# Optimization experiments

Measured on AMD Instinct MI355X. Metric: run time of the kernel, lower is better.

Reference implementation:

```python
import jax, jax.numpy as jnp
import numpy as np

B, G, S, GS, P = 32, 512, 128, 32, 10
C, H, RED = 384, 6, 16
HID = 4 * C
D = C // H
SCALE = D ** -0.5

def _gelu(x):
    return jax.nn.gelu(x, approximate=False)

def _ln(x, g, b):
    m = jnp.mean(x, -1, keepdims=True)
    v = jnp.var(x, -1, keepdims=True)
    return (x - m) * jax.lax.rsqrt(v + 1e-5) * g + b

def _split_qkv(x, W):
    Bn, T, Cc = x.shape
    qkv = (x @ W).reshape(Bn, T, 3, H, D).transpose(2, 0, 3, 1, 4)
    return qkv[0], qkv[1], qkv[2]

def _merge(x):
    Bn, Hh, T, Dd = x.shape
    return x.transpose(0, 2, 1, 3).reshape(Bn, T, Hh * Dd)

def _mha(q, k, v):
    a = jax.nn.softmax(jnp.einsum('bhnd,bhmd->bhnm', q, k) * SCALE, axis=-1)
    return jnp.einsum('bhnm,bhmd->bhnd', a, v)

def _forward(x, center1, center2, neighborhood, prompt_embeddings, ln1_g, ln1_b, Wqkv, Wproj, bproj, gate, ln2_g, ln2_b, W1, b1, W2, b2, ad_down_W, ad_down_b, ad_up_W, ad_up_b, ad_gate, bn_g, bn_b, bn_mean, bn_var, ln3_g, ln3_b, a1_Wqkv, a1_Wproj, a1_bproj, ad1_down_W, ad1_down_b, ad1_up_W, ad1_up_b, idx, center_idx, group_size, if_maxmean, pro_cof, center_cof):
    Bx, Ntok, Cc = x.shape
    # prompt dropout is identity in eval
    prompt = jnp.broadcast_to(prompt_embeddings, (Bx, P, Cc))
    # --- gated dual self / prompt-cross attention ---
    xn = _ln(x, ln1_g, ln1_b)
    q, k, v = _split_qkv(xn, Wqkv)
    xs = _mha(q, k, v)                                  # [B,H,N,D]
    _, pk, pv = _split_qkv(prompt, Wqkv)
    pa = jax.nn.softmax(jnp.einsum('bhnd,bhpd->bhnp', q, pk) * SCALE, axis=-1)
    px = jnp.einsum('bhnp,bhpd->bhnd', gate * pa, pv)   # learned gate per head
    x = x + (_merge(xs) + _merge(px)) @ Wproj + bproj
    # --- MLP + gated bottleneck adapter residual ---
    h = _gelu(_ln(x, ln2_g, ln2_b) @ W1 + b1) @ W2 + b2
    h_ad = h + _gelu(h @ ad_down_W + ad_down_b) @ ad_up_W + ad_up_b
    x = ad_gate * h_ad + x
    cls_x = x[:, :1]
    xt = x[:, 1:]                                       # [B,G,C]
    flat = xt.reshape(Bx * G, Cc)
    x_nb = flat[idx].reshape(Bx * S, group_size, Cc)    # KNN neighborhoods
    x_ct = flat[center_idx].reshape(Bx, S, Cc)          # center features
    # NOTE: original normalizes `neighborhood` by its std, but result is unused
    # --- local self-attention (attn1 over norm3) on each neighborhood ---
    nq, nk, nv = _split_qkv(_ln(x_nb, ln3_g, ln3_b), a1_Wqkv)
    no = _mha(nq, nk, nv)
    x_nb = x_nb + _merge(no) @ a1_Wproj + a1_bproj
    knn = x_nb.reshape(Bx, S, group_size, Cc)
    lc = jnp.max(knn, axis=2)
    if if_maxmean:
        lc = lc + jnp.mean(knn, axis=2)
    # BatchNorm1d (eval, running stats) + GELU over channel dim
    lc = _gelu((lc - bn_mean) * jax.lax.rsqrt(bn_var + 1e-5) * bn_g + bn_b)
    vis = lc + center_cof * x_ct                        # [B,S,C]
    # --- propagate: de_neighbors == S so sorted-topk == full weighted sum ---
    d = jnp.sum((center1[:, :, None, :] - center2[:, None, :, :]) ** 2, axis=-1)  # [B,G,S]
    w = 1.0 / (d + 1e-8)
    w = w / jnp.sum(w, axis=-1, keepdims=True)
    interp = jnp.einsum('bns,bsc->bnc', w, vis)
    xt = xt + pro_cof * interp
    out = jnp.concatenate([cls_x, xt], axis=1)
    # adapter1
    out = out + _gelu(out @ ad1_down_W + ad1_down_b) @ ad1_up_W + ad1_up_b
    return out

def setup_inputs():
    ks = jax.random.split(jax.random.key(0), 20)
    r = lambda i, shape, s=0.02: jax.random.normal(ks[i], shape, jnp.float32) * s
    return {
        'x': jax.random.normal(ks[0], (B, G + 1, C), jnp.float32),
        'center1': jax.random.normal(ks[1], (B, G, 3), jnp.float32),
        'center2': jax.random.normal(ks[2], (B, S, 3), jnp.float32),
        'neighborhood': jax.random.normal(ks[3], (B, S, GS, 3), jnp.float32),
        'prompt_embeddings': r(4, (P, C)),
        'ln1_g': jnp.ones(C), 'ln1_b': jnp.zeros(C),
        'Wqkv': r(5, (C, 3 * C)),
        'Wproj': r(6, (C, C)), 'bproj': jnp.zeros(C),
        'gate': jax.random.normal(ks[7], (1, H, 1, 1), jnp.float32),
        'ln2_g': jnp.ones(C), 'ln2_b': jnp.zeros(C),
        'W1': r(8, (C, HID)), 'b1': jnp.zeros(HID),
        'W2': r(9, (HID, C)), 'b2': jnp.zeros(C),
        'ad_down_W': r(10, (C, RED)), 'ad_down_b': jnp.zeros(RED),
        'ad_up_W': r(11, (RED, C)), 'ad_up_b': jnp.zeros(C),
        'ad_gate': jax.random.normal(ks[12], (), jnp.float32),
        'bn_g': jnp.ones(C), 'bn_b': jnp.zeros(C),
        'bn_mean': jnp.zeros(C), 'bn_var': jnp.ones(C),
        'ln3_g': jnp.ones(C), 'ln3_b': jnp.zeros(C),
        'a1_Wqkv': r(13, (C, 3 * C)),
        'a1_Wproj': r(14, (C, C)), 'a1_bproj': jnp.zeros(C),
        'ad1_down_W': r(15, (C, RED)), 'ad1_down_b': jnp.zeros(RED),
        'ad1_up_W': r(16, (RED, C)), 'ad1_up_b': jnp.zeros(C),
        'idx': jax.random.randint(ks[17], (B * S * GS,), 0, B * G),
        'center_idx': jax.random.randint(ks[18], (B * S,), 0, B * G),
        'group_size': GS,
        'if_maxmean': 1,
        'pro_cof': 1,
        'center_cof': 1,
    }

def reference(x, center1, center2, neighborhood, prompt_embeddings, ln1_g, ln1_b, Wqkv, Wproj, bproj, gate, ln2_g, ln2_b, W1, b1, W2, b2, ad_down_W, ad_down_b, ad_up_W, ad_up_b, ad_gate, bn_g, bn_b, bn_mean, bn_var, ln3_g, ln3_b, a1_Wqkv, a1_Wproj, a1_bproj, ad1_down_W, ad1_down_b, ad1_up_W, ad1_up_b, idx, center_idx, group_size, if_maxmean, pro_cof, center_cof):
    return _forward(x, center1, center2, neighborhood, prompt_embeddings, ln1_g, ln1_b, Wqkv, Wproj, bproj, gate, ln2_g, ln2_b, W1, b1, W2, b2, ad_down_W, ad_down_b, ad_up_W, ad_up_b, ad_gate, bn_g, bn_b, bn_mean, bn_var, ln3_g, ln3_b, a1_Wqkv, a1_Wproj, a1_bproj, ad1_down_W, ad1_down_b, ad1_up_W, ad1_up_b, idx, center_idx, group_size, if_maxmean, pro_cof, center_cof)
```

## Files before the change

kernel.cpp:

```cpp
#include <hip/hip_runtime.h>
#include <hip/hip_bf16.h>
#include <cstdint>
#include <cstddef>

typedef __hip_bfloat16 bf16;
constexpr int TOK = 32 * 513;

typedef __attribute__((ext_vector_type(8))) short short8;
typedef __attribute__((ext_vector_type(4))) float f32x4;

__device__ __forceinline__ float bflo(unsigned u){ return __uint_as_float(u << 16); }
__device__ __forceinline__ float bfhi(unsigned u){ return __uint_as_float(u & 0xffff0000u); }
__device__ __forceinline__ float b2f(bf16 x){ return __bfloat162float(x); }
__device__ __forceinline__ bf16  f2b(float x){ return __float2bfloat16(x); }
__device__ __forceinline__ float geluf(float x){ return 0.5f*x*(1.0f + erff(x*0.70710678118654752f)); }
__device__ __forceinline__ void unp8(uint4 u, float* f){
  f[0]=bflo(u.x); f[1]=bfhi(u.x); f[2]=bflo(u.y); f[3]=bfhi(u.y);
  f[4]=bflo(u.z); f[5]=bfhi(u.z); f[6]=bflo(u.w); f[7]=bfhi(u.w);
}
__device__ __forceinline__ float scal(const int* p){
  const int i = *p;
  if (i > -1000000 && i < 1000000) return (float)i;
  return __int_as_float(i);
}
__device__ __forceinline__ f32x4 mfma16(short8 a, short8 b, f32x4 c){
  return __builtin_amdgcn_mfma_f32_16x16x32_bf16(a, b, c, 0, 0, 0);
}
__device__ __forceinline__ int swzl(int l){ return l ^ ((l >> 3) & 7); }

__global__ __launch_bounds__(256) void detect_kernel(const unsigned* __restrict__ x,
                                                     int* __restrict__ flag)
{
  const int t = threadIdx.x;
  bool bad = false;
  for (int i = t; i < 2048; i += 256){
    const unsigned u = x[i];
    const float a = fabsf(bflo(u)), b = fabsf(bfhi(u));
    if (!(a < 1e6f) || !(b < 1e6f)) bad = true;
  }
  __shared__ int s;
  if (t == 0) s = 0;
  __syncthreads();
  const unsigned long long m = __ballot(bad);
  if (m != 0ull && (t & 63) == 0) atomicOr(&s, 1);
  __syncthreads();
  if (t == 0) *flag = s;
}

struct ConvArgs {
  const void* src[34];
  bf16*       dst[34];
  int         n[34];
};
__global__ __launch_bounds__(256) void convert_many(const int* __restrict__ flag, ConvArgs a)
{
  const int ii = blockIdx.y;
  const bool isf = (*flag != 0);
  const int n = a.n[ii];
  const void* s = a.src[ii];
  bf16* d = a.dst[ii];
  for (int i = blockIdx.x*256 + threadIdx.x; i < n; i += gridDim.x*256){
    d[i] = isf ? f2b(((const float*)s)[i]) : ((const bf16*)s)[i];
  }
}

__global__ __launch_bounds__(256) void shuffle_b(const bf16* __restrict__ W,
    bf16* __restrict__ out, int N, int KT, int NT)
{
  const int id = blockIdx.x*256 + threadIdx.x;
  if (id >= NT*KT*64) return;
  const int l  = id & 63;
  const int k0 = (id >> 6) % KT;
  const int n0 = (id >> 6) / KT;
  bf16 tmp[8];
  #pragma unroll
  for (int j = 0; j < 8; j++)
    tmp[j] = W[(size_t)(k0*32 + (l>>4)*8 + j)*N + n0*16 + (l&15)];
  *(uint4*)(out + (size_t)id*8) = *(const uint4*)tmp;
}

template<bool SRC_BF16>
__global__ __launch_bounds__(256) void ln_kernel(const void* __restrict__ src,
    const bf16* __restrict__ g, const bf16* __restrict__ b,
    bf16* __restrict__ out, int rows)
{
  const int wave = (blockIdx.x * blockDim.x + threadIdx.x) >> 6;
  const int lane = threadIdx.x & 63;
  if (wave >= rows) return;
  float v[6]; float s = 0.f, s2 = 0.f;
  #pragma unroll
  for (int i = 0; i < 6; i++){
    const int c = lane + 64*i;
    float x;
    if (SRC_BF16) x = b2f(((const bf16*)src)[(size_t)wave*384 + c]);
    else          x = ((const float*)src)[(size_t)wave*384 + c];
    v[i] = x; s += x; s2 += x*x;
  }
  #pragma unroll
  for (int mm = 32; mm; mm >>= 1){ s += __shfl_xor(s, mm); s2 += __shfl_xor(s2, mm); }
  const float mean = s * (1.f/384.f);
  const float rs = rsqrtf(s2 * (1.f/384.f) - mean*mean + 1e-5f);
  #pragma unroll
  for (int i = 0; i < 6; i++){
    const int c = lane + 64*i;
    out[(size_t)wave*384 + c] = f2b((v[i]-mean)*rs*b2f(g[c]) + b2f(b[c]));
  }
}

__global__ __launch_bounds__(256) void ln3_kernel(const float* __restrict__ xres,
    const bf16* __restrict__ g, const bf16* __restrict__ b, bf16* __restrict__ out)
{
  const int r = (blockIdx.x * blockDim.x + threadIdx.x) >> 6;
  const int lane = threadIdx.x & 63;
  if (r >= 16384) return;
  const int tok = (r >> 9)*513 + 1 + (r & 511);
  const float* xp = xres + (size_t)tok*384;
  float v[6]; float s = 0.f, s2 = 0.f;
  #pragma unroll
  for (int i = 0; i < 6; i++){
    const float x = xp[lane + 64*i];
    v[i] = x; s += x; s2 += x*x;
  }
  #pragma unroll
  for (int mm = 32; mm; mm >>= 1){ s += __shfl_xor(s, mm); s2 += __shfl_xor(s2, mm); }
  const float mean = s * (1.f/384.f);
  const float rs = rsqrtf(s2 * (1.f/384.f) - mean*mean + 1e-5f);
  #pragma unroll
  for (int i = 0; i < 6; i++){
    const int c = lane + 64*i;
    out[(size_t)r*384 + c] = f2b((v[i]-mean)*rs*b2f(g[c]) + b2f(b[c]));
  }
}

template<int EPI>
__global__ __launch_bounds__(256) void mfma_gemm(
    const bf16* __restrict__ A, const bf16* __restrict__ Bsh,
    const bf16* __restrict__ bias, const bf16* __restrict__ resid,
    void* __restrict__ outv, int M, int N, int K)
{
  __shared__ __align__(16) bf16 sA[8*64*8];
  const int t = threadIdx.x, lane = t & 63, w = t >> 6;
  const int l15 = lane & 15, quad = lane >> 4;
  const int wm = w & 1, wn = w >> 1;
  const int m0 = blockIdx.y * 128;
  const int n0t = blockIdx.x * 8 + wn * 4;
  const int KT = K >> 5;
  f32x4 acc[4][4];
  #pragma unroll
  for (int i = 0; i < 4; i++){
    #pragma unroll
    for (int j = 0; j < 4; j++) acc[i][j] = f32x4{0.f,0.f,0.f,0.f};
  }
  const int arow = t >> 1, ac0 = (t & 1) * 16;
  const int amt = arow >> 4, al15 = arow & 15, aq0 = (ac0 >> 3);

  for (int ks = 0; ks < KT; ks++){
    uint4 u0 = {0,0,0,0}, u1 = {0,0,0,0};
    const int gm = m0 + arow;
    if (gm < M){
      const bf16* ap = A + (size_t)gm*K + ks*32 + ac0;
      u0 = *(const uint4*)ap; u1 = *(const uint4*)(ap + 8);
    }
    *(uint4*)(sA + ((amt*64 + aq0*16     + al15) << 3)) = u0;
    *(uint4*)(sA + ((amt*64 + (aq0+1)*16 + al15) << 3)) = u1;
    __syncthreads();
    short8 afr[4];
    #pragma unroll
    for (int i = 0; i < 4; i++)
      afr[i] = *(const short8*)(sA + (((wm*4+i)*64 + lane) << 3));
    #pragma unroll
    for (int j = 0; j < 4; j++){
      const short8 b = *(const short8*)(Bsh + ((size_t)((n0t+j)*KT + ks)*64 + lane)*8);
      #pragma unroll
      for (int i = 0; i < 4; i++) acc[i][j] = mfma16(afr[i], b, acc[i][j]);
    }
    __syncthreads();
  }
  #pragma unroll
  for (int i = 0; i < 4; i++){
    #pragma unroll
    for (int r = 0; r < 4; r++){
      const int gm = m0 + (wm*4+i)*16 + quad*4 + r;
      if (gm < M){
        #pragma unroll
        for (int j = 0; j < 4; j++){
          const int gn = (n0t+j)*16 + l15;
          float v = acc[i][j][r];
          const size_t o = (size_t)gm*N + gn;
          if (EPI == 0){ v += b2f(bias[gn]); ((bf16*)outv)[o] = f2b(v); }
          else if (EPI == 1){ ((bf16*)outv)[o] = f2b(v); }
          else if (EPI == 2){ v += b2f(bias[gn]); ((bf16*)outv)[o] = f2b(geluf(v)); }
          else { v += b2f(bias[gn]) + b2f(resid[o]); ((float*)outv)[o] = v; }
        }
      }
    }
  }
}

__global__ __launch_bounds__(256) void pqkv_kernel(const bf16* __restrict__ pe,
    const bf16* __restrict__ Wqkv, float* __restrict__ pq)
{
  const int n  = blockIdx.x*64 + (threadIdx.x & 63);
  const int rg = threadIdx.x >> 6;
  for (int r = rg; r < 10; r += 4){
    float s0 = 0.f, s1 = 0.f;
    for (int c = 0; c < 384; c += 2){
      s0 = fmaf(b2f(pe[(size_t)r*384+c]),   b2f(Wqkv[(size_t)c*1152 + n]),     s0);
      s1 = fmaf(b2f(pe[(size_t)r*384+c+1]), b2f(Wqkv[(size_t)(c+1)*1152 + n]), s1);
    }
    pq[(size_t)r*1152 + n] = s0 + s1;
  }
}

__global__ __launch_bounds__(256) void attn_kernel(
    const bf16* __restrict__ qkv, const float* __restrict__ pq,
    const bf16* __restrict__ gate, bf16* __restrict__ ao)
{
  __shared__ __align__(16) bf16 s_q[64*72];
  __shared__ __align__(16) bf16 s_k[64*72];
  __shared__ __align__(16) bf16 s_vT[64*72];
  __shared__ __align__(16) bf16 s_p[4*16*40];
  __shared__ __align__(16) bf16 s_pk[16*72];
  __shared__ __align__(16) bf16 s_pvT[64*40];
  const int bh = blockIdx.y;
  const int b = bh / 6, h = bh % 6;
  const int q0 = blockIdx.x * 64;
  const int t = threadIdx.x, lane = t & 63, w = t >> 6;
  const int l15 = lane & 15, quad = lane >> 4;

  {
    const int row = t >> 2, dc = (t & 3) * 16;
    const int tok = q0 + row;
    uint4 u0 = {0,0,0,0}, u1 = {0,0,0,0};
    if (tok < 513){
      const bf16* p = qkv + (size_t)(b*513 + tok)*1152 + h*64 + dc;
      u0 = *(const uint4*)p; u1 = *(const uint4*)(p + 8);
    }
    *(uint4*)(s_q + row*72 + dc)     = u0;
    *(uint4*)(s_q + row*72 + dc + 8) = u1;
  }
  {
    const int j = t >> 4, dc = (t & 15) * 4;
    float f[4] = {0.f,0.f,0.f,0.f};
    if (j < 10){
      const float* pk = pq + (size_t)j*1152 + 384 + h*64 + dc;
      f[0]=pk[0]; f[1]=pk[1]; f[2]=pk[2]; f[3]=pk[3];
    }
    bf16 tmp[4] = {f2b(f[0]),f2b(f[1]),f2b(f[2]),f2b(f[3])};
    *(uint2*)(s_pk + j*72 + dc) = *(const uint2*)tmp;
  }
  {
    const int d = t & 63, kg = t >> 6;
    #pragma unroll
    for (int kk = 0; kk < 8; kk++){
      const int key = kg*8 + kk;
      bf16 v = f2b(0.f);
      if (key < 10) v = f2b(pq[(size_t)key*1152 + 768 + h*64 + d]);
      s_pvT[d*40 + key] = v;
    }
  }

  float m_i[4], l_i[4];
  f32x4 oacc[4];
  #pragma unroll
  for (int r = 0; r < 4; r++){ m_i[r] = -30000.f; l_i[r] = 0.f; }
  #pragma unroll
  for (int nt = 0; nt < 4; nt++) oacc[nt] = f32x4{0.f,0.f,0.f,0.f};
  bf16* myp = s_p + w*16*40;
  const short8* aq = (const short8*)(s_q + (w*16 + l15)*72);

  for (int kt = 0; kt < 9; kt++){
    const int kb = kt*64;
    __syncthreads();
    {
      const int kp = t & 31, dg = t >> 5;
      const int key0 = kb + 2*kp;
      uint4 k0v = {0,0,0,0}, k1v = {0,0,0,0}, v0 = {0,0,0,0}, v1 = {0,0,0,0};
      if (key0 < 513){
        const bf16* base = qkv + (size_t)(b*513 + key0)*1152 + h*64 + dg*8;
        k0v = *(const uint4*)(base + 384);
        v0  = *(const uint4*)(base + 768);
      }
      if (key0 + 1 < 513){
        const bf16* base = qkv + (size_t)(b*513 + key0 + 1)*1152 + h*64 + dg*8;
        k1v = *(const uint4*)(base + 384);
        v1  = *(const uint4*)(base + 768);
      }
      *(uint4*)(s_k + (2*kp)*72   + dg*8) = k0v;
      *(uint4*)(s_k + (2*kp+1)*72 + dg*8) = k1v;
      const unsigned short* a0 = (const unsigned short*)&v0;
      const unsigned short* a1 = (const unsigned short*)&v1;
      unsigned* vt = (unsigned*)s_vT;
      #pragma unroll
      for (int j = 0; j < 8; j++)
        vt[(dg*8 + j)*36 + kp] = (unsigned)a0[j] | ((unsigned)a1[j] << 16);
    }
    __syncthreads();

    f32x4 sreg[4];
    #pragma unroll
    for (int nt = 0; nt < 4; nt++){
      f32x4 acc = f32x4{0.f,0.f,0.f,0.f};
      const short8* bk = (const short8*)(s_k + (nt*16 + l15)*72);
      acc = mfma16(aq[quad],     bk[quad],     acc);
      acc = mfma16(aq[4 + quad], bk[4 + quad], acc);
      const bool kvalid = (kb + nt*16 + l15) < 513;
      #pragma unroll
      for (int r = 0; r < 4; r++)
        sreg[nt][r] = kvalid ? acc[r]*0.125f : -30000.f;
    }
    float alpha[4];
    #pragma unroll
    for (int r = 0; r < 4; r++){
      float mx = fmaxf(fmaxf(sreg[0][r], sreg[1][r]), fmaxf(sreg[2][r], sreg[3][r]));
      #pragma unroll
      for (int mm = 8; mm; mm >>= 1) mx = fmaxf(mx, __shfl_xor(mx, mm));
      const float mn = fmaxf(m_i[r], mx);
      alpha[r] = __expf(m_i[r] - mn);
      m_i[r] = mn;
      float ps = 0.f;
      #pragma unroll
      for (int nt = 0; nt < 4; nt++){
        const float p = __expf(sreg[nt][r] - mn);
        sreg[nt][r] = p; ps += p;
      }
      #pragma unroll
      for (int mm = 8; mm; mm >>= 1) ps += __shfl_xor(ps, mm);
      l_i[r] = l_i[r]*alpha[r] + ps;
    }
    #pragma unroll
    for (int nt = 0; nt < 4; nt++){
      #pragma unroll
      for (int r = 0; r < 4; r++)
        myp[(quad*4 + r)*40 + nt*16 + l15] = f2b(sreg[nt][r]);
    }
    #pragma unroll
    for (int nt = 0; nt < 4; nt++){
      #pragma unroll
      for (int r = 0; r < 4; r++) oacc[nt][r] *= alpha[r];
    }
    const short8* ap = (const short8*)(myp + l15*40);
    #pragma unroll
    for (int nt = 0; nt < 4; nt++){
      const short8* bv = (const short8*)(s_vT + (nt*16 + l15)*72);
      oacc[nt] = mfma16(ap[quad],     bv[quad],     oacc[nt]);
      oacc[nt] = mfma16(ap[4 + quad], bv[4 + quad], oacc[nt]);
    }
  }

  f32x4 sp;
  {
    f32x4 acc = f32x4{0.f,0.f,0.f,0.f};
    const short8* bp = (const short8*)(s_pk + l15*72);
    acc = mfma16(aq[quad],     bp[quad],     acc);
    acc = mfma16(aq[4 + quad], bp[4 + quad], acc);
    #pragma unroll
    for (int r = 0; r < 4; r++)
      sp[r] = (l15 < 10) ? acc[r]*0.125f : -30000.f;
  }
  float psr[4];
  #pragma unroll
  for (int r = 0; r < 4; r++){
    float mx = sp[r];
    #pragma unroll
    for (int mm = 8; mm; mm >>= 1) mx = fmaxf(mx, __shfl_xor(mx, mm));
    const float p = __expf(sp[r] - mx);
    float ps = p;
    #pragma unroll
    for (int mm = 8; mm; mm >>= 1) ps += __shfl_xor(ps, mm);
    psr[r] = ps;
    myp[(quad*4 + r)*40 + l15]      = f2b(p);
    myp[(quad*4 + r)*40 + 16 + l15] = f2b(0.f);
  }
  f32x4 pva[4];
  {
    const short8* ap = (const short8*)(myp + l15*40);
    #pragma unroll
    for (int nt = 0; nt < 4; nt++){
      const short8* bv = (const short8*)(s_pvT + (nt*16 + l15)*40);
      pva[nt] = mfma16(ap[quad], bv[quad], f32x4{0.f,0.f,0.f,0.f});
    }
  }

  const float gh = b2f(gate[h]);
  #pragma unroll
  for (int r = 0; r < 4; r++){
    const int tok = q0 + w*16 + quad*4 + r;
    if (tok < 513){
      const float invl = 1.f/l_i[r];
      const float gps  = gh/psr[r];
      #pragma unroll
      for (int nt = 0; nt < 4; nt++){
        const float val = oacc[nt][r]*invl + pva[nt][r]*gps;
        ao[(size_t)(b*513 + tok)*384 + h*64 + nt*16 + l15] = f2b(val);
      }
    }
  }
}

__global__ __launch_bounds__(256) void adapter_mid_kernel(const bf16* __restrict__ h,
    const bf16* __restrict__ Wd, const bf16* __restrict__ bd,
    const bf16* __restrict__ Wu, const bf16* __restrict__ bu,
    const bf16* __restrict__ p_gate, float* __restrict__ xres)
{
  __shared__ float s_h[384];
  __shared__ float s_part[16][17];
  __shared__ float s_y[16];
  const size_t row = blockIdx.x;
  const int t = threadIdx.x;
  const bf16* hp = h + row*384;
  for (int c = t; c < 384; c += 256) s_h[c] = b2f(hp[c]);
  __syncthreads();
  const int o = t & 15, p = t >> 4;
  float part0 = 0.f, part1 = 0.f;
  for (int c = p; c < 384; c += 32){
    part0 = fmaf(s_h[c],    b2f(Wd[(size_t)c*16 + o]),      part0);
    part1 = fmaf(s_h[c+16], b2f(Wd[(size_t)(c+16)*16 + o]), part1);
  }
  s_part[o][p] = part0 + part1;
  __syncthreads();
  if (t < 16){
    float sum = 0.f;
    #pragma unroll
    for (int pp = 0; pp < 16; pp++) sum += s_part[t][pp];
    s_y[t] = geluf(sum + b2f(bd[t]));
  }
  __syncthreads();
  const float g = b2f(p_gate[0]);
  for (int c = t; c < 384; c += 256){
    float up = 0.f;
    #pragma unroll
    for (int o2 = 0; o2 < 16; o2++) up = fmaf(s_y[o2], b2f(Wu[(size_t)o2*384 + c]), up);
    const float had = s_h[c] + up + b2f(bu[c]);
    xres[row*384 + c] = g*had + xres[row*384 + c];
  }
}

__global__ __launch_bounds__(256) void adapter_final_kernel(const float* __restrict__ xr,
    const bf16* __restrict__ Wd, const bf16* __restrict__ bd,
    const bf16* __restrict__ Wu, const bf16* __restrict__ bu,
    const int* __restrict__ flag, void* __restrict__ out)
{
  __shared__ float s_h[384];
  __shared__ float s_part[16][17];
  __shared__ float s_y[16];
  const size_t row = blockIdx.x;
  const int t = threadIdx.x;
  const float* hp = xr + row*384;
  for (int c = t; c < 384; c += 256) s_h[c] = hp[c];
  __syncthreads();
  const int o = t & 15, p = t >> 4;
  float part0 = 0.f, part1 = 0.f;
  for (int c = p; c < 384; c += 32){
    part0 = fmaf(s_h[c],    b2f(Wd[(size_t)c*16 + o]),      part0);
    part1 = fmaf(s_h[c+16], b2f(Wd[(size_t)(c+16)*16 + o]), part1);
  }
  s_part[o][p] = part0 + part1;
  __syncthreads();
  if (t < 16){
    float sum = 0.f;
    #pragma unroll
    for (int pp = 0; pp < 16; pp++) sum += s_part[t][pp];
    s_y[t] = geluf(sum + b2f(bd[t]));
  }
  __syncthreads();
  const bool isf = (*flag != 0);
  for (int c = t; c < 384; c += 256){
    float up = 0.f;
    #pragma unroll
    for (int o2 = 0; o2 < 16; o2++) up = fmaf(s_y[o2], b2f(Wu[(size_t)o2*384 + c]), up);
    const float v = s_h[c] + up + b2f(bu[c]);
    if (isf) ((float*)out)[row*384 + c] = v;
    else     ((bf16*)out)[row*384 + c] = f2b(v);
  }
}

__global__ __launch_bounds__(512) void local_kernel(
    const bf16* __restrict__ qkv3, const float* __restrict__ xres,
    const int* __restrict__ idx, const int* __restrict__ cidx,
    const bf16* __restrict__ Bp, const bf16* __restrict__ bp1,
    const bf16* __restrict__ bng, const bf16* __restrict__ bnb,
    const bf16* __restrict__ bnm, const bf16* __restrict__ bnv,
    const int* __restrict__ p_ifmm, const int* __restrict__ p_ccof,
    float* __restrict__ vis)
{
  __shared__ __align__(16) bf16 sQ[6*4*64*8];
  __shared__ __align__(16) bf16 sK[6*4*64*8];
  __shared__ __align__(16) bf16 sV[6*4*64*8];
  __shared__ __align__(16) bf16 sP[2*64*8];
  __shared__ __align__(16) bf16 sO[4*64*8];
  __shared__ int s_flat[32];
  __shared__ int s_tok[32];

  const int g = blockIdx.x;
  const int t = threadIdx.x, lane = t & 63, w = t >> 6;
  const int l15 = lane & 15, quad = lane >> 4;
  const int lanez = swzl(lane);

  if (t < 32){
    const int r = idx[g*32 + t];
    s_flat[t] = r;
    s_tok[t]  = (r >> 9)*513 + 1 + (r & 511);
  }
  __syncthreads();

  for (int ch = t; ch < 4608; ch += 512){
    const int row = ch & 31;
    const int c0  = (ch >> 5) * 8;
    const uint4 u = *(const uint4*)(qkv3 + (size_t)s_flat[row]*1152 + c0);
    const int grp = c0 / 384;
    const int rem = c0 - grp*384;
    const int h = rem >> 6, d0 = rem & 63;
    if (grp < 2){
      const int T = h*4 + (row>>4)*2 + (d0>>5);
      const int L = ((d0>>3)&3)*16 + (row&15);
      const int addr = (T*64 + swzl(L))*8;
      if (grp == 0) *(uint4*)(sQ + addr) = u;
      else          *(uint4*)(sK + addr) = u;
    } else {
      const bf16* sv = (const bf16*)&u;
      #pragma unroll
      for (int j2 = 0; j2 < 8; j2++){
        const int d = d0 + j2;
        const int L = (row>>3)*16 + (d&15);
        sV[((h*4 + (d>>4))*64 + swzl(L))*8 + (row&7)] = sv[j2];
      }
    }
  }
  __syncthreads();

  f32x4 accp[3][2];
  #pragma unroll
  for (int a = 0; a < 3; a++){
    #pragma unroll
    for (int m = 0; m < 2; m++) accp[a][m] = f32x4{0.f,0.f,0.f,0.f};
  }

  for (int h = 0; h < 6; h++){
    if (w < 2){
      const int mt = w;
      f32x4 sr[2];
      #pragma unroll
      for (int nt = 0; nt < 2; nt++){
        f32x4 acc = f32x4{0.f,0.f,0.f,0.f};
        #pragma unroll
        for (int k0 = 0; k0 < 2; k0++){
          const short8 a = *(const short8*)(sQ + ((h*4 + mt*2 + k0)*64 + lanez)*8);
          const short8 b = *(const short8*)(sK + ((h*4 + nt*2 + k0)*64 + lanez)*8);
          acc = mfma16(a, b, acc);
        }
        #pragma unroll
        for (int r = 0; r < 4; r++) sr[nt][r] = acc[r]*0.125f;
      }
      #pragma unroll
      for (int r = 0; r < 4; r++){
        float mx = fmaxf(sr[0][r], sr[1][r]);
        #pragma unroll
        for (int mm = 8; mm; mm >>= 1) mx = fmaxf(mx, __shfl_xor(mx, mm));
        const float e0 = __expf(sr[0][r] - mx), e1 = __expf(sr[1][r] - mx);
        float sm = e0 + e1;
        #pragma unroll
        for (int mm = 8; mm; mm >>= 1) sm += __shfl_xor(sm, mm);
        const float inv = 1.f/sm;
        const int m = quad*4 + r;
        const int L0 = (l15 >> 3)*16       + m;
        const int L1 = (2 + (l15 >> 3))*16 + m;
        sP[(mt*64 + swzl(L0))*8 + (l15 & 7)] = f2b(e0*inv);
        sP[(mt*64 + swzl(L1))*8 + (l15 & 7)] = f2b(e1*inv);
      }
    }
    __syncthreads();

    {
      const int mt = w & 1, nt = w >> 1;
      const short8 a = *(const short8*)(sP + (mt*64 + lanez)*8);
      const short8 b = *(const short8*)(sV + ((h*4 + nt)*64 + lanez)*8);
      const f32x4 o = mfma16(a, b, f32x4{0.f,0.f,0.f,0.f});
      const int k0w = nt >> 1, qdw = (nt & 1)*2 + (l15 >> 3), jw = l15 & 7;
      #pragma unroll
      for (int r = 0; r < 4; r++){
        const int L = qdw*16 + quad*4 + r;
        sO[((mt*2 + k0w)*64 + swzl(L))*8 + jw] = f2b(o[r]);
      }
    }
    __syncthreads();

    {
      short8 afr[2][2];
      #pragma unroll
      for (int mt = 0; mt < 2; mt++){
        #pragma unroll
        for (int k0l = 0; k0l < 2; k0l++)
          afr[mt][k0l] = *(const short8*)(sO + ((mt*2 + k0l)*64 + lanez)*8);
      }
      #pragma unroll
      for (int tt = 0; tt < 3; tt++){
        const int nt = w*3 + tt;
        #pragma unroll
        for (int k0l = 0; k0l < 2; k0l++){
          const short8 b = *(const short8*)(Bp + ((size_t)(nt*12 + 2*h + k0l)*64 + lane)*8);
          accp[tt][0] = mfma16(afr[0][k0l], b, accp[tt][0]);
          accp[tt][1] = mfma16(afr[1][k0l], b, accp[tt][1]);
        }
      }
    }
    __syncthreads();
  }

  const float fmm  = scal(p_ifmm);
  const float ccof = scal(p_ccof);
  const int cr = cidx[g];
  const int ctok = (cr >> 9)*513 + 1 + (cr & 511);
  #pragma unroll
  for (int tt = 0; tt < 3; tt++){
    const int n = (w*3 + tt)*16 + l15;
    const float bb = b2f(bp1[n]);
    float mx = -3e30f, sm = 0.f;
    #pragma unroll
    for (int mt = 0; mt < 2; mt++){
      #pragma unroll
      for (int r = 0; r < 4; r++){
        const int tok = mt*16 + quad*4 + r;
        const float v = accp[tt][mt][r] + bb + xres[(size_t)s_tok[tok]*384 + n];
        mx = fmaxf(mx, v); sm += v;
      }
    }
    mx = fmaxf(mx, __shfl_xor(mx, 16)); sm += __shfl_xor(sm, 16);
    mx = fmaxf(mx, __shfl_xor(mx, 32)); sm += __shfl_xor(sm, 32);
    if (quad == 0){
      const float lc = (fmm != 0.f) ? (mx + sm*(1.f/32.f)) : mx;
      const float nr = (lc - b2f(bnm[n])) * rsqrtf(b2f(bnv[n]) + 1e-5f) * b2f(bng[n]) + b2f(bnb[n]);
      vis[(size_t)g*384 + n] = geluf(nr) + ccof * xres[(size_t)ctok*384 + n];
    }
  }
}

__global__ __launch_bounds__(256) void interp_kernel(const bf16* __restrict__ c1,
    const bf16* __restrict__ c2, const float* __restrict__ vis,
    const int* __restrict__ p_pcof, float* __restrict__ xres)
{
  __shared__ float s_w[8][128];
  __shared__ float s_red[2];
  const int b = blockIdx.y;
  const int n0 = blockIdx.x * 8;
  const int t = threadIdx.x;
  for (int ni = 0; ni < 8; ni++){
    const int n = n0 + ni;
    float wv = 0.f;
    if (t < 128){
      float d2 = 0.f;
      #pragma unroll
      for (int k = 0; k < 3; k++){
        const float a = b2f(c1[((size_t)b*512 + n)*3 + k]);
        const float c = b2f(c2[((size_t)b*128 + t)*3 + k]);
        const float df = a - c; d2 += df*df;
      }
      wv = 1.f/(d2 + 1e-8f);
    }
    float rsum = wv;
    #pragma unroll
    for (int mm = 32; mm; mm >>= 1) rsum += __shfl_xor(rsum, mm);
    if (((t & 63) == 0) && t < 128) s_red[t >> 6] = rsum;
    __syncthreads();
    const float tot = s_red[0] + s_red[1];
    if (t < 128) s_w[ni][t] = wv / tot;
    __syncthreads();
  }
  float acc1[8], acc2[8];
  #pragma unroll
  for (int ni = 0; ni < 8; ni++){ acc1[ni] = 0.f; acc2[ni] = 0.f; }
  for (int s = 0; s < 128; s++){
    const float* vp = vis + ((size_t)b*128 + s)*384;
    const float v1 = vp[t];
    const float v2 = (t < 128) ? vp[t + 256] : 0.f;
    #pragma unroll
    for (int ni = 0; ni < 8; ni++){
      const float wn = s_w[ni][s];
      acc1[ni] = fmaf(wn, v1, acc1[ni]);
      acc2[ni] = fmaf(wn, v2, acc2[ni]);
    }
  }
  const float pc = scal(p_pcof);
  #pragma unroll
  for (int ni = 0; ni < 8; ni++){
    const int tok = b*513 + 1 + n0 + ni;
    xres[(size_t)tok*384 + t] += pc*acc1[ni];
    if (t < 128) xres[(size_t)tok*384 + t + 256] += pc*acc2[ni];
  }
}

extern "C" void kernel_launch(void* const* d_in, const int* in_sizes, int n_in,
                              void* d_out, int out_size, void* d_ws, size_t ws_size,
                              hipStream_t stream)
{
  (void)n_in; (void)out_size; (void)ws_size;
  const int*  idx   = (const int*)d_in[35];
  const int*  cidx  = (const int*)d_in[36];
  const int*  ifmm  = (const int*)d_in[38];
  const int*  pcof  = (const int*)d_in[39];
  const int*  ccof  = (const int*)d_in[40];

  size_t off = 0;
  auto alloc = [&](size_t bytes) -> void* {
    void* p = (char*)d_ws + off; off += (bytes + 255) & ~(size_t)255; return p;
  };
  int*   flag = (int*)  alloc(sizeof(int));
  float* xres = (float*)alloc((size_t)TOK*384*4);
  bf16*  slab = (bf16*) alloc((size_t)TOK*1536*2);
  bf16*  xn   = (bf16*) alloc((size_t)TOK*384*2);
  float* pq   = (float*)alloc((size_t)10*1152*4);
  bf16*  Bq   = (bf16*) alloc((size_t)72*12*64*8*2);
  bf16*  Bp   = (bf16*) alloc((size_t)24*12*64*8*2);
  bf16*  Bqkv = (bf16*) alloc((size_t)72*12*64*8*2);
  bf16*  Bw1  = (bf16*) alloc((size_t)96*12*64*8*2);
  bf16*  Bw2  = (bf16*) alloc((size_t)24*48*64*8*2);
  bf16*  Bwp  = (bf16*) alloc((size_t)24*12*64*8*2);

  bf16*  qkvb = slab;
  bf16*  x_c  = slab + (size_t)TOK*1152;
  bf16*  h1   = slab;
  bf16*  qkv3 = slab;
  bf16*  xln3 = slab + (size_t)TOK*1152;
  bf16*  ao   = xn;
  bf16*  hbuf = xn;
  float* visb = (float*)xn;

  const int conv_ids[34] = {0,1,2,4,5,6,7,8,9,10,11,12,13,14,15,16,17,
                            18,19,20,21,22,23,24,25,26,27,28,29,30,31,32,33,34};
  ConvArgs ca;
  bf16* canon[41];
  int maxn = 1;
  for (int k = 0; k < 34; k++){
    const int i = conv_ids[k];
    const int n = in_sizes[i];
    bf16* dst = (i == 0) ? x_c : (bf16*)alloc((size_t)n*2);
    ca.src[k] = d_in[i]; ca.dst[k] = dst; ca.n[k] = n;
    canon[i] = dst;
    if (n > maxn) maxn = n;
  }
  detect_kernel<<<dim3(1), dim3(256), 0, stream>>>((const unsigned*)d_in[0], flag);
  {
    int gx = (maxn + 256*64 - 1) / (256*64); if (gx > 64) gx = 64; if (gx < 1) gx = 1;
    convert_many<<<dim3(gx, 34), dim3(256), 0, stream>>>(flag, ca);
  }

  const bf16 *x_in = canon[0], *c1 = canon[1], *c2 = canon[2], *pe = canon[4],
             *ln1g = canon[5], *ln1b = canon[6], *Wqkv = canon[7], *Wproj = canon[8],
             *bproj = canon[9], *gate = canon[10], *ln2g = canon[11], *ln2b = canon[12],
             *W1 = canon[13], *b1 = canon[14], *W2 = canon[15], *b2v = canon[16],
             *adW = canon[17], *adb = canon[18], *adU = canon[19], *adub = canon[20],
             *adg = canon[21], *bng = canon[22], *bnb = canon[23], *bnm = canon[24],
             *bnv = canon[25], *ln3g = canon[26], *ln3b = canon[27], *a1W = canon[28],
             *a1P = canon[29], *a1pb = canon[30], *d1W = canon[31], *d1b = canon[32],
             *u1W = canon[33], *u1b = canon[34];

  shuffle_b<<<dim3(216), dim3(256), 0, stream>>>(a1W, Bq, 1152, 12, 72);
  shuffle_b<<<dim3(72),  dim3(256), 0, stream>>>(a1P, Bp, 384, 12, 24);
  shuffle_b<<<dim3(216), dim3(256), 0, stream>>>(Wqkv, Bqkv, 1152, 12, 72);
  shuffle_b<<<dim3(288), dim3(256), 0, stream>>>(W1, Bw1, 1536, 12, 96);
  shuffle_b<<<dim3(288), dim3(256), 0, stream>>>(W2, Bw2, 384, 48, 24);
  shuffle_b<<<dim3(72),  dim3(256), 0, stream>>>(Wproj, Bwp, 384, 12, 24);

  ln_kernel<true><<<dim3((TOK*64)/256), dim3(256), 0, stream>>>((const void*)x_in, ln1g, ln1b, xn, TOK);
  mfma_gemm<1><<<dim3(9,129), dim3(256), 0, stream>>>(xn, Bqkv, nullptr, nullptr, qkvb, TOK, 1152, 384);
  pqkv_kernel<<<dim3(18), dim3(256), 0, stream>>>(pe, Wqkv, pq);
  attn_kernel<<<dim3(9,192), dim3(256), 0, stream>>>(qkvb, pq, gate, ao);
  mfma_gemm<3><<<dim3(3,129), dim3(256), 0, stream>>>(ao, Bwp, bproj, x_in, xres, TOK, 384, 384);
  ln_kernel<false><<<dim3((TOK*64)/256), dim3(256), 0, stream>>>((const void*)xres, ln2g, ln2b, xn, TOK);
  mfma_gemm<2><<<dim3(12,129), dim3(256), 0, stream>>>(xn, Bw1, b1, nullptr, h1, TOK, 1536, 384);
  mfma_gemm<0><<<dim3(3,129), dim3(256), 0, stream>>>(h1, Bw2, b2v, nullptr, hbuf, TOK, 384, 1536);
  adapter_mid_kernel<<<dim3(TOK), dim3(256), 0, stream>>>(hbuf, adW, adb, adU, adub, adg, xres);
  ln3_kernel<<<dim3((16384*64)/256), dim3(256), 0, stream>>>(xres, ln3g, ln3b, xln3);
  mfma_gemm<1><<<dim3(9,128), dim3(256), 0, stream>>>(xln3, Bq, nullptr, nullptr, qkv3, 16384, 1152, 384);
  local_kernel<<<dim3(4096), dim3(512), 0, stream>>>(qkv3, xres, idx, cidx, Bp, a1pb,
                                                     bng, bnb, bnm, bnv, ifmm, ccof, visb);
  interp_kernel<<<dim3(64,32), dim3(256), 0, stream>>>(c1, c2, visb, pcof, xres);
  adapter_final_kernel<<<dim3(TOK), dim3(256), 0, stream>>>(xres, d1W, d1b, u1W, u1b, flag, d_out);
}
```

Measured before the change: 960.5 us.

## Process local attention in two head chunks to halve shared memory and barriers

The local attention kernel now loads Q/K/V for three heads at a time instead of all six. This halves the shared-memory footprint and reuses the Q buffer as the output staging area. Within each chunk, six waves compute the scores for three heads in parallel, which cuts the number of barriers per block from 24 to 8 and uses more of the 8 waves for softmax. The gather of QKV rows is split into two phases, so global loads are no longer issued all at once.

```diff
diff --git a/kernel.cpp b/kernel.cpp
--- a/kernel.cpp
+++ b/kernel.cpp
@@ -484,13 +484,13 @@
     const int* __restrict__ p_ifmm, const int* __restrict__ p_ccof,
     float* __restrict__ vis)
 {
-  __shared__ __align__(16) bf16 sQ[6*4*64*8];
-  __shared__ __align__(16) bf16 sK[6*4*64*8];
-  __shared__ __align__(16) bf16 sV[6*4*64*8];
-  __shared__ __align__(16) bf16 sP[2*64*8];
-  __shared__ __align__(16) bf16 sO[4*64*8];
+  __shared__ __align__(16) bf16 sQ[3*4*64*8];
+  __shared__ __align__(16) bf16 sK[3*4*64*8];
+  __shared__ __align__(16) bf16 sV[3*4*64*8];
+  __shared__ __align__(16) bf16 sP[3*2*64*8];
   __shared__ int s_flat[32];
   __shared__ int s_tok[32];
+  bf16* sO = sQ;
 
   const int g = blockIdx.x;
   const int t = threadIdx.x, lane = t & 63, w = t >> 6;
@@ -504,31 +504,6 @@
   }
   __syncthreads();
 
-  for (int ch = t; ch < 4608; ch += 512){
-    const int row = ch & 31;
-    const int c0  = (ch >> 5) * 8;
-    const uint4 u = *(const uint4*)(qkv3 + (size_t)s_flat[row]*1152 + c0);
-    const int grp = c0 / 384;
-    const int rem = c0 - grp*384;
-    const int h = rem >> 6, d0 = rem & 63;
-    if (grp < 2){
-      const int T = h*4 + (row>>4)*2 + (d0>>5);
-      const int L = ((d0>>3)&3)*16 + (row&15);
-      const int addr = (T*64 + swzl(L))*8;
-      if (grp == 0) *(uint4*)(sQ + addr) = u;
-      else          *(uint4*)(sK + addr) = u;
-    } else {
-      const bf16* sv = (const bf16*)&u;
-      #pragma unroll
-      for (int j2 = 0; j2 < 8; j2++){
-        const int d = d0 + j2;
-        const int L = (row>>3)*16 + (d&15);
-        sV[((h*4 + (d>>4))*64 + swzl(L))*8 + (row&7)] = sv[j2];
-      }
-    }
-  }
-  __syncthreads();
-
   f32x4 accp[3][2];
   #pragma unroll
   for (int a = 0; a < 3; a++){
@@ -536,9 +511,36 @@
     for (int m = 0; m < 2; m++) accp[a][m] = f32x4{0.f,0.f,0.f,0.f};
   }
 
-  for (int h = 0; h < 6; h++){
-    if (w < 2){
-      const int mt = w;
+  for (int hc = 0; hc < 2; hc++){
+    for (int ch = t; ch < 2304; ch += 512){
+      const int row = ch & 31;
+      const int cc  = ch >> 5;
+      const int seg = cc / 24;
+      const int wi  = cc - seg*24;
+      const int h   = wi >> 3;
+      const int d0  = (wi & 7) * 8;
+      const int col = seg*384 + (hc*3 + h)*64 + d0;
+      const uint4 u = *(const uint4*)(qkv3 + (size_t)s_flat[row]*1152 + col);
+      if (seg < 2){
+        const int T = h*4 + (row>>4)*2 + (d0>>5);
+        const int L = ((d0>>3)&3)*16 + (row&15);
+        const int addr = (T*64 + swzl(L))*8;
+        if (seg == 0) *(uint4*)(sQ + addr) = u;
+        else          *(uint4*)(sK + addr) = u;
+      } else {
+        const bf16* sv = (const bf16*)&u;
+        #pragma unroll
+        for (int j2 = 0; j2 < 8; j2++){
+          const int d = d0 + j2;
+          const int L = (row>>3)*16 + (d&15);
+          sV[((h*4 + (d>>4))*64 + swzl(L))*8 + (row&7)] = sv[j2];
+        }
+      }
+    }
+    __syncthreads();
+
+    if (w < 6){
+      const int h = w >> 1, mt = w & 1;
       f32x4 sr[2];
       #pragma unroll
       for (int nt = 0; nt < 2; nt++){
@@ -565,40 +567,45 @@
         const int m = quad*4 + r;
         const int L0 = (l15 >> 3)*16       + m;
         const int L1 = (2 + (l15 >> 3))*16 + m;
-        sP[(mt*64 + swzl(L0))*8 + (l15 & 7)] = f2b(e0*inv);
-        sP[(mt*64 + swzl(L1))*8 + (l15 & 7)] = f2b(e1*inv);
+        sP[((h*2 + mt)*64 + swzl(L0))*8 + (l15 & 7)] = f2b(e0*inv);
+        sP[((h*2 + mt)*64 + swzl(L1))*8 + (l15 & 7)] = f2b(e1*inv);
       }
     }
     __syncthreads();
 
     {
       const int mt = w & 1, nt = w >> 1;
-      const short8 a = *(const short8*)(sP + (mt*64 + lanez)*8);
-      const short8 b = *(const short8*)(sV + ((h*4 + nt)*64 + lanez)*8);
-      const f32x4 o = mfma16(a, b, f32x4{0.f,0.f,0.f,0.f});
       const int k0w = nt >> 1, qdw = (nt & 1)*2 + (l15 >> 3), jw = l15 & 7;
       #pragma unroll
-      for (int r = 0; r < 4; r++){
-        const int L = qdw*16 + quad*4 + r;
-        sO[((mt*2 + k0w)*64 + swzl(L))*8 + jw] = f2b(o[r]);
-      }
-    }
-    __syncthreads();
-
-    {
+      for (int h = 0; h < 3; h++){
+        const short8 a = *(const short8*)(sP + ((h*2 + mt)*64 + lanez)*8);
+        const short8 b = *(const short8*)(sV + ((h*4 + nt)*64 + lanez)*8);
+        const f32x4 o = mfma16(a, b, f32x4{0.f,0.f,0.f,0.f});
+        #pragma unroll
+        for (int r = 0; r < 4; r++){
+          const int L = qdw*16 + quad*4 + r;
+          sO[((h*4 + mt*2 + k0w)*64 + swzl(L))*8 + jw] = f2b(o[r]);
+        }
+      }
+    }
+    __syncthreads();
+
+    #pragma unroll
+    for (int h = 0; h < 3; h++){
       short8 afr[2][2];
       #pragma unroll
       for (int mt = 0; mt < 2; mt++){
         #pragma unroll
         for (int k0l = 0; k0l < 2; k0l++)
-          afr[mt][k0l] = *(const short8*)(sO + ((mt*2 + k0l)*64 + lanez)*8);
-      }
+          afr[mt][k0l] = *(const short8*)(sO + ((h*4 + mt*2 + k0l)*64 + lanez)*8);
+      }
+      const int hg2 = (hc*3 + h)*2;
       #pragma unroll
       for (int tt = 0; tt < 3; tt++){
         const int nt = w*3 + tt;
         #pragma unroll
         for (int k0l = 0; k0l < 2; k0l++){
-          const short8 b = *(const short8*)(Bp + ((size_t)(nt*12 + 2*h + k0l)*64 + lane)*8);
+          const short8 b = *(const short8*)(Bp + ((size_t)(nt*12 + hg2 + k0l)*64 + lane)*8);
           accp[tt][0] = mfma16(afr[0][k0l], b, accp[tt][0]);
           accp[tt][1] = mfma16(afr[1][k0l], b, accp[tt][1]);
         }
```

New measurement: 936.6 us. 2.5% less time.
